# Performance work log

Measured on AMD Instinct MI355X. Metric: run time of the kernel, lower is better.

The kernel has to match this reference:

```python
import jax, jax.numpy as jnp
import numpy as np
import math

HIDDEN = 1024
N_HEADS = 16
HEAD = HIDDEN // N_HEADS

def setup_inputs() -> dict:
    key = jax.random.key(0)
    k1, k2, k3 = jax.random.split(key, 3)
    encodings = jax.random.normal(k1, (2, 2048, HIDDEN), dtype=jnp.float32)
    W_attn = jax.random.normal(k2, (HIDDEN, 3 * HIDDEN), dtype=jnp.float32) * 0.02
    b_attn = jnp.zeros((3 * HIDDEN,), dtype=jnp.float32)
    W_out = jax.random.normal(k3, (HIDDEN, HIDDEN), dtype=jnp.float32) * 0.02
    b_out = jnp.zeros((HIDDEN,), dtype=jnp.float32)
    return {"encodings": encodings, "W_attn": W_attn, "b_attn": b_attn,
            "W_out": W_out, "b_out": b_out}

def reference(encodings, W_attn, b_attn, W_out, b_out):
    b, n, _ = encodings.shape
    qkv = encodings @ W_attn + b_attn              # [b, n, 3*hidden]
    q, k, v = jnp.split(qkv, 3, axis=-1)
    # 'b n (h l) -> b h n l'
    def to_heads(t):
        return t.reshape(b, n, N_HEADS, HEAD).transpose(0, 2, 1, 3)
    q, k, v = to_heads(q), to_heads(k), to_heads(v)
    # scores[b,h,k,q]; causal mask keeps key_pos <= query_pos
    scores = jnp.einsum('bhki,bhqi->bhkq', k, q) / math.sqrt(HEAD)
    mask = jnp.arange(n)[:, None] <= jnp.arange(n)[None, :]   # [k, q]
    scores = jnp.where(mask, scores, jnp.float32(-10000.0))
    attn = jax.nn.softmax(scores, axis=2)          # softmax over key dim
    combined = jnp.einsum('bhkq,bhkl->bhql', attn, v)  # [b, h, n, head]
    out = combined.transpose(0, 2, 1, 3).reshape(b, n, HIDDEN)
    return out @ W_out + b_out
```

## Files before the change

kernel.cpp:

```cpp
#include <hip/hip_runtime.h>
#include <hip/hip_bf16.h>

typedef __attribute__((ext_vector_type(8))) short bf16x8;
typedef __attribute__((ext_vector_type(4))) short bf16x4;
typedef __attribute__((ext_vector_type(4))) float f32x4;

__device__ __forceinline__ short f2bf(float f) {
    unsigned u = __float_as_uint(f);
    u += 0x7fff + ((u >> 16) & 1);
    return (short)(u >> 16);
}
__device__ __forceinline__ float bf2f(short s) {
    return __uint_as_float(((unsigned)(unsigned short)s) << 16);
}
__device__ __forceinline__ unsigned pk_bf16(float lo, float hi) {
    __hip_bfloat162 t = __float22bfloat162_rn(make_float2(lo, hi));
    unsigned u;
    __builtin_memcpy(&u, &t, 4);
    return u;
}

#define GLOAD_LDS16(gp, lp)                                                            \
    __builtin_amdgcn_global_load_lds(                                                  \
        (const __attribute__((address_space(1))) unsigned*)(gp),                       \
        (__attribute__((address_space(3))) unsigned*)(lp), 16, 0, 0)

#define QK_SCALE 0.180336879f
#define MFMA16(a, b, c) __builtin_amdgcn_mfma_f32_16x16x32_bf16((a), (b), (c), 0, 0, 0)

__device__ __forceinline__ void tcvt_tile(const float* __restrict__ W, short* __restrict__ Wt,
                                          int K, int N, int bx, int by, int t,
                                          short (*tile)[72]) {
    const int k0 = by * 64, n0 = bx * 64;
    #pragma unroll
    for (int jj = 0; jj < 4; ++jj) {
        int row = jj * 16 + (t >> 4);
        int col = (t & 15) * 4;
        f32x4 v = *(const f32x4*)&W[(size_t)(k0 + row) * N + n0 + col];
        bf16x4 b = {f2bf(v.x), f2bf(v.y), f2bf(v.z), f2bf(v.w)};
        *(bf16x4*)&tile[row][col] = b;
    }
    __syncthreads();
    const int nr = t >> 2, kc = (t & 3) * 16;
    bf16x8 o0, o1;
    #pragma unroll
    for (int j = 0; j < 8; ++j) { o0[j] = tile[kc + j][nr]; o1[j] = tile[kc + 8 + j][nr]; }
    short* dst = &Wt[(size_t)(n0 + nr) * K + k0 + kc];
    *(bf16x8*)dst = o0;
    *(bf16x8*)(dst + 8) = o1;
}

__global__ __launch_bounds__(256) void prep_kernel(
    const float* __restrict__ enc, const float* __restrict__ Wa,
    const float* __restrict__ ba, const float* __restrict__ Wo,
    const float* __restrict__ bo, short* __restrict__ Abf,
    short* __restrict__ WtA, short* __restrict__ bbA,
    short* __restrict__ WtO, short* __restrict__ bbO)
{
    __shared__ alignas(16) short tile[64][72];
    const int id = blockIdx.x, t = threadIdx.x;
    if (id < 2048) {
        const int i = id * 2048 + t * 8;
        f32x4 a = *(const f32x4*)&enc[i];
        f32x4 b = *(const f32x4*)&enc[i + 4];
        bf16x8 o = {f2bf(a.x), f2bf(a.y), f2bf(a.z), f2bf(a.w),
                    f2bf(b.x), f2bf(b.y), f2bf(b.z), f2bf(b.w)};
        *(bf16x8*)&Abf[i] = o;
    } else if (id == 2048) {
        for (int j = t * 8; j < 3072; j += 2048) {
            f32x4 a = *(const f32x4*)&ba[j];
            f32x4 b = *(const f32x4*)&ba[j + 4];
            bf16x8 o = {f2bf(a.x), f2bf(a.y), f2bf(a.z), f2bf(a.w),
                        f2bf(b.x), f2bf(b.y), f2bf(b.z), f2bf(b.w)};
            *(bf16x8*)&bbA[j] = o;
        }
    } else if (id == 2049) {
        if (t < 128) {
            const int j = t * 8;
            f32x4 a = *(const f32x4*)&bo[j];
            f32x4 b = *(const f32x4*)&bo[j + 4];
            bf16x8 o = {f2bf(a.x), f2bf(a.y), f2bf(a.z), f2bf(a.w),
                        f2bf(b.x), f2bf(b.y), f2bf(b.z), f2bf(b.w)};
            *(bf16x8*)&bbO[j] = o;
        }
        __syncthreads();
    } else if (id < 2818) {
        const int lid = id - 2050;
        tcvt_tile(Wa, WtA, 1024, 3072, lid % 48, lid / 48, t, tile);
    } else {
        const int lid = id - 2818;
        tcvt_tile(Wo, WtO, 1024, 1024, lid % 16, lid / 16, t, tile);
    }
}

template<int BN, bool F32OUT, bool SPLIT3>
__global__ __launch_bounds__(256) void gemm_bt(
    const short* __restrict__ A, const short* __restrict__ Bt,
    const short* __restrict__ bias, void* __restrict__ C,
    short* __restrict__ Kw, short* __restrict__ Vw, int M, int N, int K)
{
    __shared__ alignas(16) short LB[128 * 64 + BN * 64];
    short* As = LB;
    short* Bs = LB + 128 * 64;
    short* Ct = LB;

    const int tid = threadIdx.x, w = tid >> 6, lane = tid & 63;
    const int quad = lane >> 4, l16 = lane & 15;
    constexpr int MT = (BN == 128) ? 4 : 2;
    const int wm = (BN == 128) ? (w >> 1) : w;
    const int wn = (BN == 128) ? (w & 1) : 0;
    const int m0 = blockIdx.y * 128, n0 = blockIdx.x * BN;
    const int srow = lane >> 3;
    const int scol = ((lane & 7) ^ srow) * 8;

    f32x4 acc[MT][4] = {};

    for (int k0 = 0; k0 < K; k0 += 64) {
        __syncthreads();
        #pragma unroll
        for (int jj = 0; jj < 4; ++jj) {
            const int rb = w * 32 + jj * 8;
            GLOAD_LDS16(&A[(size_t)(m0 + rb + srow) * K + k0 + scol], &As[rb * 64]);
        }
        if (BN == 128) {
            #pragma unroll
            for (int jj = 0; jj < 4; ++jj) {
                const int rb = w * 32 + jj * 8;
                GLOAD_LDS16(&Bt[(size_t)(n0 + rb + srow) * K + k0 + scol], &Bs[rb * 64]);
            }
        } else {
            #pragma unroll
            for (int jj = 0; jj < 2; ++jj) {
                const int rb = w * 16 + jj * 8;
                GLOAD_LDS16(&Bt[(size_t)(n0 + rb + srow) * K + k0 + scol], &Bs[rb * 64]);
            }
        }
        __syncthreads();
        #pragma unroll
        for (int half = 0; half < 2; ++half) {
            const int kc2 = half * 4 + quad;
            bf16x8 af[MT], bfr[4];
            #pragma unroll
            for (int i = 0; i < MT; ++i) {
                const int row = wm * (MT * 16) + i * 16 + l16;
                af[i] = *(const bf16x8*)&As[row * 64 + ((kc2 ^ (row & 7)) << 3)];
            }
            #pragma unroll
            for (int i = 0; i < 4; ++i) {
                const int row = wn * 64 + i * 16 + l16;
                bfr[i] = *(const bf16x8*)&Bs[row * 64 + ((kc2 ^ (row & 7)) << 3)];
            }
            #pragma unroll
            for (int mt = 0; mt < MT; ++mt)
                #pragma unroll
                for (int nt = 0; nt < 4; ++nt)
                    acc[mt][nt] = MFMA16(af[mt], bfr[nt], acc[mt][nt]);
        }
    }

    if (SPLIT3) {
        const int g = n0 >> 10;
        const int lc0 = n0 & 1023;
        __syncthreads();
        if (g < 2) {
            #pragma unroll
            for (int nt = 0; nt < 4; ++nt) {
                const int col = wn * 64 + nt * 16 + l16;
                const float bv = bf2f(bias[n0 + col]);
                const int chunk = col >> 3, wi = col & 7;
                #pragma unroll
                for (int mt = 0; mt < 4; ++mt) {
                    const int rbase = wm * 64 + mt * 16 + quad * 4;
                    #pragma unroll
                    for (int r = 0; r < 4; ++r) {
                        const int row = rbase + r;
                        float v = acc[mt][nt][r] + bv;
                        if (g == 0) v *= QK_SCALE;
                        Ct[row * 128 + (((chunk ^ (row & 15)) << 3) | wi)] = f2bf(v);
                    }
                }
            }
        } else {
            #pragma unroll
            for (int nt = 0; nt < 4; ++nt) {
                const int d = wn * 64 + nt * 16 + l16;
                const float bv = bf2f(bias[n0 + d]);
                const int dsw = d & 15;
                #pragma unroll
                for (int mt = 0; mt < 4; ++mt) {
                    const int key0 = wm * 64 + mt * 16 + quad * 4;
                    bf16x4 p = {f2bf(acc[mt][nt][0] + bv), f2bf(acc[mt][nt][1] + bv),
                                f2bf(acc[mt][nt][2] + bv), f2bf(acc[mt][nt][3] + bv)};
                    *(bf16x4*)&Ct[d * 128 + ((((key0 >> 3) ^ dsw) << 3) | (key0 & 7))] = p;
                }
            }
        }
        __syncthreads();
        const int batch = m0 >> 11;
        const int kc0 = (m0 & 2047) >> 6;
        const int head0 = lc0 >> 6;
        if (g == 0) {
            short* dst = (short*)C;
            #pragma unroll
            for (int i = 0; i < 8; ++i) {
                const int idx = i * 256 + tid;
                const int row = idx >> 4, chunk = idx & 15;
                bf16x8 v = *(const bf16x8*)&Ct[row * 128 + ((chunk ^ (row & 15)) << 3)];
                *(bf16x8*)&dst[(size_t)(m0 + row) * 1024 + lc0 + chunk * 8] = v;
            }
        } else if (g == 1) {
            #pragma unroll
            for (int i = 0; i < 8; ++i) {
                const int idx = i * 256 + tid;
                const int qd = idx >> 9, c = idx & 511;
                const int kcL = qd >> 1, headL = qd & 1;
                const int s = c >> 7, h2 = (c >> 6) & 1;
                const int l16c = c & 15, quadc = (c >> 4) & 3;
                const int row = kcL * 64 + s * 16 + l16c;
                const int colc = headL * 8 + h2 * 4 + quadc;
                bf16x8 v = *(const bf16x8*)&Ct[row * 128 + ((colc ^ (row & 15)) << 3)];
                const int bh = batch * 16 + head0 + headL, kc = kc0 + kcL;
                *(bf16x8*)&Kw[((size_t)(bh * 32 + kc) * 512 + c) * 8] = v;
            }
        } else {
            #pragma unroll
            for (int i = 0; i < 8; ++i) {
                const int idx = i * 256 + tid;
                const int qd = idx >> 9, c = idx & 511;
                const int kcL = qd >> 1, headL = qd & 1;
                const int h2 = c >> 8, dt = (c >> 6) & 3;
                const int l16c = c & 15, quadc = (c >> 4) & 3;
                const int d = headL * 64 + dt * 16 + l16c;
                const int keyc = kcL * 8 + h2 * 4 + quadc;
                bf16x8 v = *(const bf16x8*)&Ct[d * 128 + ((keyc ^ (d & 15)) << 3)];
                const int bh = batch * 16 + head0 + headL, kc = kc0 + kcL;
                *(bf16x8*)&Vw[((size_t)(bh * 32 + kc) * 512 + c) * 8] = v;
            }
        }
    } else {
        #pragma unroll
        for (int nt = 0; nt < 4; ++nt) {
            const int col = n0 + wn * 64 + nt * 16 + l16;
            const float bv = bf2f(bias[col]);
            #pragma unroll
            for (int mt = 0; mt < MT; ++mt) {
                const int row = m0 + wm * (MT * 16) + mt * 16 + quad * 4;
                #pragma unroll
                for (int r = 0; r < 4; ++r) {
                    float v = acc[mt][nt][r] + bv;
                    if (F32OUT) ((float*)C)[(size_t)(row + r) * N + col] = v;
                    else        ((short*)C)[(size_t)(row + r) * N + col] = f2bf(v);
                }
            }
        }
    }
}

__global__ __launch_bounds__(256) void attn_kernel(
    const short* __restrict__ Qw, const short* __restrict__ Kx,
    const short* __restrict__ Vx, short* __restrict__ comb)
{
    __shared__ alignas(16) short KV[3][2][4096];
    __shared__ alignas(16) short Ps[4][2][16 * 72];

    const int tid = threadIdx.x, w4 = tid >> 6, lane = tid & 63;
    const int p = w4 >> 1;
    const int w = w4 & 1;
    const int quad = lane >> 4, l16 = lane & 15;
    const int bh = blockIdx.x;
    const int g = blockIdx.y;
    const int tA = 2 * g + p, tB = 63 - tA;
    const int batch = bh >> 4, head = bh & 15;
    const size_t rowbase = (size_t)batch * 2048;
    const int hcol = head * 64;
    const int q0A = tA * 32 + w * 16, q0B = tB * 32 + w * 16;
    const int diagA = g;
    const int maxD = 31 - g;
    const short* Kxbh = Kx + (size_t)bh * 131072;
    const short* Vxbh = Vx + (size_t)bh * 131072;
    const int lofs = lane * 8;
    short* pwA = &Ps[w4][0][0];
    short* pwB = &Ps[w4][1][0];

    bf16x8 qfA[2], qfB[2];
    {
        const short* pa = &Qw[(rowbase + q0A + l16) * 1024 + hcol];
        const short* pb = &Qw[(rowbase + q0B + l16) * 1024 + hcol];
        qfA[0] = *(const bf16x8*)(pa + quad * 8);
        qfA[1] = *(const bf16x8*)(pa + 32 + quad * 8);
        qfB[0] = *(const bf16x8*)(pb + quad * 8);
        qfB[1] = *(const bf16x8*)(pb + 32 + quad * 8);
    }
    asm volatile("s_waitcnt vmcnt(0)" ::: "memory");

    f32x4 otA[4] = {}, otB[4] = {};
    float laccA = 0.f, laccB = 0.f;

    const int sbase = w4 * 64;

    #define STAGE_KV(kcs, buf)                                                              \
        do {                                                                                \
            const size_t nb_ = (size_t)(kcs)*4096;                                          \
            _Pragma("unroll")                                                               \
            for (int j = 0; j < 2; ++j) {                                                   \
                GLOAD_LDS16(&Kxbh[nb_ + (size_t)(j * 256 + sbase + lane) * 8],              \
                            &KV[buf][0][(j * 256 + sbase) * 8]);                            \
                GLOAD_LDS16(&Vxbh[nb_ + (size_t)(j * 256 + sbase + lane) * 8],              \
                            &KV[buf][1][(j * 256 + sbase) * 8]);                            \
            }                                                                               \
        } while (0)

    STAGE_KV(0, 0);
    STAGE_KV(1, 1);
    asm volatile("s_waitcnt vmcnt(4)" ::: "memory");
    __builtin_amdgcn_s_barrier();
    __builtin_amdgcn_sched_barrier(0);

    int cur = 0;
    for (int kc = 0; kc <= maxD; ++kc) {
        const bool actA = (kc <= diagA);
        const int key0 = kc * 64;

        {
            const int ks = (kc + 2 <= maxD) ? kc + 2 : maxD;
            const int wb = (cur + 2 >= 3) ? cur - 1 : cur + 2;
            STAGE_KV(ks, wb);
        }

        bf16x8 kf[4][2];
        #pragma unroll
        for (int s = 0; s < 4; ++s) {
            kf[s][0] = *(const bf16x8*)&KV[cur][0][(s * 2 + 0) * 512 + lofs];
            kf[s][1] = *(const bf16x8*)&KV[cur][0][(s * 2 + 1) * 512 + lofs];
        }

        f32x4 svA[4], svB[4];
        #pragma unroll
        for (int s = 0; s < 4; ++s) {
            f32x4 a = {0.f, 0.f, 0.f, 0.f};
            a = MFMA16(kf[s][0], qfB[0], a);
            a = MFMA16(kf[s][1], qfB[1], a);
            svB[s] = a;
            if (actA) {
                f32x4 b = {0.f, 0.f, 0.f, 0.f};
                b = MFMA16(kf[s][0], qfA[0], b);
                b = MFMA16(kf[s][1], qfA[1], b);
                svA[s] = b;
            }
        }

        bf16x8 vf[2][4];
        #pragma unroll
        for (int hh = 0; hh < 2; ++hh)
            #pragma unroll
            for (int dt = 0; dt < 4; ++dt)
                vf[hh][dt] = *(const bf16x8*)&KV[cur][1][(hh * 4 + dt) * 512 + lofs];

        if (kc == maxD) {
            const int qq = q0B + l16;
            #pragma unroll
            for (int s = 0; s < 4; ++s) {
                const int keyb = key0 + s * 16 + quad * 4;
                #pragma unroll
                for (int r = 0; r < 4; ++r)
                    svB[s][r] = (keyb + r <= qq) ? svB[s][r] : -1e30f;
            }
        }
        #pragma unroll
        for (int s = 0; s < 4; ++s) {
            #pragma unroll
            for (int r = 0; r < 4; ++r) svB[s][r] = exp2f(svB[s][r]);
            laccB += (svB[s][0] + svB[s][1]) + (svB[s][2] + svB[s][3]);
            *(unsigned*)&pwB[l16 * 72 + s * 16 + quad * 4]     = pk_bf16(svB[s][0], svB[s][1]);
            *(unsigned*)&pwB[l16 * 72 + s * 16 + quad * 4 + 2] = pk_bf16(svB[s][2], svB[s][3]);
        }
        if (actA) {
            if (kc == diagA) {
                const int qq = q0A + l16;
                #pragma unroll
                for (int s = 0; s < 4; ++s) {
                    const int keyb = key0 + s * 16 + quad * 4;
                    #pragma unroll
                    for (int r = 0; r < 4; ++r)
                        svA[s][r] = (keyb + r <= qq) ? svA[s][r] : -1e30f;
                }
            }
            #pragma unroll
            for (int s = 0; s < 4; ++s) {
                #pragma unroll
                for (int r = 0; r < 4; ++r) svA[s][r] = exp2f(svA[s][r]);
                laccA += (svA[s][0] + svA[s][1]) + (svA[s][2] + svA[s][3]);
                *(unsigned*)&pwA[l16 * 72 + s * 16 + quad * 4]     = pk_bf16(svA[s][0], svA[s][1]);
                *(unsigned*)&pwA[l16 * 72 + s * 16 + quad * 4 + 2] = pk_bf16(svA[s][2], svA[s][3]);
            }
        }

        {
            bf16x8 pfB0 = *(const bf16x8*)&pwB[l16 * 72 + quad * 8];
            bf16x8 pfB1 = *(const bf16x8*)&pwB[l16 * 72 + 32 + quad * 8];
            #pragma unroll
            for (int dt = 0; dt < 4; ++dt) {
                otB[dt] = MFMA16(vf[0][dt], pfB0, otB[dt]);
                otB[dt] = MFMA16(vf[1][dt], pfB1, otB[dt]);
            }
            if (actA) {
                bf16x8 pfA0 = *(const bf16x8*)&pwA[l16 * 72 + quad * 8];
                bf16x8 pfA1 = *(const bf16x8*)&pwA[l16 * 72 + 32 + quad * 8];
                #pragma unroll
                for (int dt = 0; dt < 4; ++dt) {
                    otA[dt] = MFMA16(vf[0][dt], pfA0, otA[dt]);
                    otA[dt] = MFMA16(vf[1][dt], pfA1, otA[dt]);
                }
            }
        }

        asm volatile("s_waitcnt vmcnt(4)" ::: "memory");
        __builtin_amdgcn_s_barrier();
        __builtin_amdgcn_sched_barrier(0);
        cur = (cur + 1 >= 3) ? 0 : cur + 1;
    }
    #undef STAGE_KV

    laccA += __shfl_xor(laccA, 16);
    laccA += __shfl_xor(laccA, 32);
    laccB += __shfl_xor(laccB, 16);
    laccB += __shfl_xor(laccB, 32);
    const float invA = 1.0f / laccA, invB = 1.0f / laccB;

    #pragma unroll
    for (int dt = 0; dt < 4; ++dt) {
        *(unsigned*)&pwA[l16 * 72 + dt * 16 + quad * 4]     = pk_bf16(otA[dt][0] * invA, otA[dt][1] * invA);
        *(unsigned*)&pwA[l16 * 72 + dt * 16 + quad * 4 + 2] = pk_bf16(otA[dt][2] * invA, otA[dt][3] * invA);
        *(unsigned*)&pwB[l16 * 72 + dt * 16 + quad * 4]     = pk_bf16(otB[dt][0] * invB, otB[dt][1] * invB);
        *(unsigned*)&pwB[l16 * 72 + dt * 16 + quad * 4 + 2] = pk_bf16(otB[dt][2] * invB, otB[dt][3] * invB);
    }
    {
        const int qr = lane >> 2, dc = (lane & 3) * 16;
        bf16x8 a0 = *(const bf16x8*)&pwA[qr * 72 + dc];
        bf16x8 a1 = *(const bf16x8*)&pwA[qr * 72 + dc + 8];
        short* dstA = &comb[(rowbase + q0A + qr) * 1024 + hcol + dc];
        *(bf16x8*)dstA = a0;
        *(bf16x8*)(dstA + 8) = a1;
        bf16x8 b0 = *(const bf16x8*)&pwB[qr * 72 + dc];
        bf16x8 b1 = *(const bf16x8*)&pwB[qr * 72 + dc + 8];
        short* dstB = &comb[(rowbase + q0B + qr) * 1024 + hcol + dc];
        *(bf16x8*)dstB = b0;
        *(bf16x8*)(dstB + 8) = b1;
    }
}

extern "C" void kernel_launch(void* const* d_in, const int* in_sizes, int n_in,
                              void* d_out, int out_size, void* d_ws, size_t ws_size,
                              hipStream_t stream)
{
    const float* enc = (const float*)d_in[0];
    const float* Wa  = (const float*)d_in[1];
    const float* ba  = (const float*)d_in[2];
    const float* Wo  = (const float*)d_in[3];
    const float* bo  = (const float*)d_in[4];
    float* out = (float*)d_out;

    char* ws = (char*)d_ws;
    short* Abf  = (short*)ws;
    short* comb = (short*)ws;
    short* WtO  = (short*)(ws + ((size_t)8 << 20));
    short* bbA  = (short*)(ws + ((size_t)10 << 20));
    short* bbO  = (short*)(ws + ((size_t)10 << 20) + 16384);
    short* WtA  = (short*)(ws + ((size_t)11 << 20));
    short* Kx   = (short*)(ws + ((size_t)17 << 20));
    short* Vx   = (short*)(ws + ((size_t)25 << 20));
    short* Qw   = (short*)(ws + ((size_t)33 << 20));

    prep_kernel<<<3074, 256, 0, stream>>>(enc, Wa, ba, Wo, bo, Abf, WtA, bbA, WtO, bbO);
    gemm_bt<128, false, true><<<dim3(24, 32), 256, 0, stream>>>(
        Abf, WtA, bbA, Qw, Kx, Vx, 4096, 3072, 1024);
    attn_kernel<<<dim3(32, 16), 256, 0, stream>>>(Qw, Kx, Vx, comb);
    gemm_bt<64, true, false><<<dim3(16, 32), 256, 0, stream>>>(
        comb, WtO, bbO, out, nullptr, nullptr, 4096, 1024, 1024);
}
```

Baseline: 189.0 us.

## Keep softmax probabilities in registers instead of an LDS round-trip for PV MFMA

Probabilities are packed to bf16 and fed straight from registers into the PV MFMA, removing the LDS write and read-back through the pw buffers. To make the register layout of P match the MFMA operand, the V staging layout written by the QKV GEMM epilogue is permuted so each 8-element key group gathers two 4-key chunks. This removes LDS traffic and waits in the attention inner loop, at the cost of slightly more scattered LDS reads in the projection epilogue.

Measured after the change: 188.1 us. Within noise of the previous version (-0.5%).

```diff
diff --git a/kernel.cpp b/kernel.cpp
--- a/kernel.cpp
+++ b/kernel.cpp
@@ -231,8 +231,11 @@
                 const int h2 = c >> 8, dt = (c >> 6) & 3;
                 const int l16c = c & 15, quadc = (c >> 4) & 3;
                 const int d = headL * 64 + dt * 16 + l16c;
-                const int keyc = kcL * 8 + h2 * 4 + quadc;
-                bf16x8 v = *(const bf16x8*)&Ct[d * 128 + ((keyc ^ (d & 15)) << 3)];
+                const int Ka = kcL * 64 + h2 * 32 + quadc * 4;
+                const int Kb = Ka + 16;
+                bf16x4 va = *(const bf16x4*)&Ct[d * 128 + (((Ka >> 3) ^ (d & 15)) << 3) + (Ka & 7)];
+                bf16x4 vb = *(const bf16x4*)&Ct[d * 128 + (((Kb >> 3) ^ (d & 15)) << 3) + (Kb & 7)];
+                bf16x8 v = {va[0], va[1], va[2], va[3], vb[0], vb[1], vb[2], vb[3]};
                 const int bh = batch * 16 + head0 + headL, kc = kc0 + kcL;
                 *(bf16x8*)&Vw[((size_t)(bh * 32 + kc) * 512 + c) * 8] = v;
             }
@@ -366,14 +369,30 @@
                     svB[s][r] = (keyb + r <= qq) ? svB[s][r] : -1e30f;
             }
         }
-        #pragma unroll
-        for (int s = 0; s < 4; ++s) {
-            #pragma unroll
-            for (int r = 0; r < 4; ++r) svB[s][r] = exp2f(svB[s][r]);
-            laccB += (svB[s][0] + svB[s][1]) + (svB[s][2] + svB[s][3]);
-            *(unsigned*)&pwB[l16 * 72 + s * 16 + quad * 4]     = pk_bf16(svB[s][0], svB[s][1]);
-            *(unsigned*)&pwB[l16 * 72 + s * 16 + quad * 4 + 2] = pk_bf16(svB[s][2], svB[s][3]);
-        }
+        {
+            unsigned uB[4][2];
+            #pragma unroll
+            for (int s = 0; s < 4; ++s) {
+                #pragma unroll
+                for (int r = 0; r < 4; ++r) svB[s][r] = exp2f(svB[s][r]);
+                laccB += (svB[s][0] + svB[s][1]) + (svB[s][2] + svB[s][3]);
+                uB[s][0] = pk_bf16(svB[s][0], svB[s][1]);
+                uB[s][1] = pk_bf16(svB[s][2], svB[s][3]);
+            }
+            bf16x8 pfB0, pfB1;
+            {
+                unsigned t0[4] = {uB[0][0], uB[0][1], uB[1][0], uB[1][1]};
+                unsigned t1[4] = {uB[2][0], uB[2][1], uB[3][0], uB[3][1]};
+                __builtin_memcpy(&pfB0, t0, 16);
+                __builtin_memcpy(&pfB1, t1, 16);
+            }
+            #pragma unroll
+            for (int dt = 0; dt < 4; ++dt) {
+                otB[dt] = MFMA16(vf[0][dt], pfB0, otB[dt]);
+                otB[dt] = MFMA16(vf[1][dt], pfB1, otB[dt]);
+            }
+        }
+
         if (actA) {
             if (kc == diagA) {
                 const int qq = q0A + l16;
@@ -385,32 +404,26 @@
                         svA[s][r] = (keyb + r <= qq) ? svA[s][r] : -1e30f;
                 }
             }
+            unsigned uA[4][2];
             #pragma unroll
             for (int s = 0; s < 4; ++s) {
                 #pragma unroll
                 for (int r = 0; r < 4; ++r) svA[s][r] = exp2f(svA[s][r]);
                 laccA += (svA[s][0] + svA[s][1]) + (svA[s][2] + svA[s][3]);
-                *(unsigned*)&pwA[l16 * 72 + s * 16 + quad * 4]     = pk_bf16(svA[s][0], svA[s][1]);
-                *(unsigned*)&pwA[l16 * 72 + s * 16 + quad * 4 + 2] = pk_bf16(svA[s][2], svA[s][3]);
-            }
-        }
-
-        {
-            bf16x8 pfB0 = *(const bf16x8*)&pwB[l16 * 72 + quad * 8];
-            bf16x8 pfB1 = *(const bf16x8*)&pwB[l16 * 72 + 32 + quad * 8];
+                uA[s][0] = pk_bf16(svA[s][0], svA[s][1]);
+                uA[s][1] = pk_bf16(svA[s][2], svA[s][3]);
+            }
+            bf16x8 pfA0, pfA1;
+            {
+                unsigned t0[4] = {uA[0][0], uA[0][1], uA[1][0], uA[1][1]};
+                unsigned t1[4] = {uA[2][0], uA[2][1], uA[3][0], uA[3][1]};
+                __builtin_memcpy(&pfA0, t0, 16);
+                __builtin_memcpy(&pfA1, t1, 16);
+            }
             #pragma unroll
             for (int dt = 0; dt < 4; ++dt) {
-                otB[dt] = MFMA16(vf[0][dt], pfB0, otB[dt]);
-                otB[dt] = MFMA16(vf[1][dt], pfB1, otB[dt]);
-            }
-            if (actA) {
-                bf16x8 pfA0 = *(const bf16x8*)&pwA[l16 * 72 + quad * 8];
-                bf16x8 pfA1 = *(const bf16x8*)&pwA[l16 * 72 + 32 + quad * 8];
-                #pragma unroll
-                for (int dt = 0; dt < 4; ++dt) {
-                    otA[dt] = MFMA16(vf[0][dt], pfA0, otA[dt]);
-                    otA[dt] = MFMA16(vf[1][dt], pfA1, otA[dt]);
-                }
+                otA[dt] = MFMA16(vf[0][dt], pfA0, otA[dt]);
+                otA[dt] = MFMA16(vf[1][dt], pfA1, otA[dt]);
             }
         }
 
```

## Repack V layout so P stays in registers; one 64-row query tile per block

Applied to the files above, without the earlier changes.

The V workspace layout written by the QKV GEMM epilogue is permuted so the exp'd score fragments can serve directly as the B operand of the PV MFMA. This removes the per-iteration LDS round-trip for P. The attention kernel also drops the paired-tile (A/B) causal load balancing in favor of 1024 blocks, each handling one 64-query tile, scheduled longest-first. The final output staging reuses the KV shared buffer, cutting LDS footprint to help occupancy, at the cost of more blocks and less K/V reuse per staged chunk.

New measurement: 178.4 us. -5.6%, faster.

```diff
diff --git a/kernel.cpp b/kernel.cpp
--- a/kernel.cpp
+++ b/kernel.cpp
@@ -231,8 +231,11 @@
                 const int h2 = c >> 8, dt = (c >> 6) & 3;
                 const int l16c = c & 15, quadc = (c >> 4) & 3;
                 const int d = headL * 64 + dt * 16 + l16c;
-                const int keyc = kcL * 8 + h2 * 4 + quadc;
-                bf16x8 v = *(const bf16x8*)&Ct[d * 128 + ((keyc ^ (d & 15)) << 3)];
+                const int Ka = kcL * 64 + h2 * 32 + quadc * 4;
+                const int Kb = Ka + 16;
+                bf16x4 va = *(const bf16x4*)&Ct[d * 128 + (((Ka >> 3) ^ (d & 15)) << 3) + (Ka & 7)];
+                bf16x4 vb = *(const bf16x4*)&Ct[d * 128 + (((Kb >> 3) ^ (d & 15)) << 3) + (Kb & 7)];
+                bf16x8 v = {va[0], va[1], va[2], va[3], vb[0], vb[1], vb[2], vb[3]};
                 const int bh = batch * 16 + head0 + headL, kc = kc0 + kcL;
                 *(bf16x8*)&Vw[((size_t)(bh * 32 + kc) * 512 + c) * 8] = v;
             }
@@ -261,40 +264,30 @@
     const short* __restrict__ Vx, short* __restrict__ comb)
 {
     __shared__ alignas(16) short KV[3][2][4096];
-    __shared__ alignas(16) short Ps[4][2][16 * 72];
 
     const int tid = threadIdx.x, w4 = tid >> 6, lane = tid & 63;
-    const int p = w4 >> 1;
-    const int w = w4 & 1;
     const int quad = lane >> 4, l16 = lane & 15;
-    const int bh = blockIdx.x;
-    const int g = blockIdx.y;
-    const int tA = 2 * g + p, tB = 63 - tA;
+    const int blk = blockIdx.x;
+    const int n = 31 - (blk >> 5);
+    const int bh = blk & 31;
     const int batch = bh >> 4, head = bh & 15;
     const size_t rowbase = (size_t)batch * 2048;
     const int hcol = head * 64;
-    const int q0A = tA * 32 + w * 16, q0B = tB * 32 + w * 16;
-    const int diagA = g;
-    const int maxD = 31 - g;
+    const int q0 = n * 64 + w4 * 16;
     const short* Kxbh = Kx + (size_t)bh * 131072;
     const short* Vxbh = Vx + (size_t)bh * 131072;
     const int lofs = lane * 8;
-    short* pwA = &Ps[w4][0][0];
-    short* pwB = &Ps[w4][1][0];
-
-    bf16x8 qfA[2], qfB[2];
+
+    bf16x8 qf[2];
     {
-        const short* pa = &Qw[(rowbase + q0A + l16) * 1024 + hcol];
-        const short* pb = &Qw[(rowbase + q0B + l16) * 1024 + hcol];
-        qfA[0] = *(const bf16x8*)(pa + quad * 8);
-        qfA[1] = *(const bf16x8*)(pa + 32 + quad * 8);
-        qfB[0] = *(const bf16x8*)(pb + quad * 8);
-        qfB[1] = *(const bf16x8*)(pb + 32 + quad * 8);
+        const short* pq = &Qw[(rowbase + q0 + l16) * 1024 + hcol];
+        qf[0] = *(const bf16x8*)(pq + quad * 8);
+        qf[1] = *(const bf16x8*)(pq + 32 + quad * 8);
     }
     asm volatile("s_waitcnt vmcnt(0)" ::: "memory");
 
-    f32x4 otA[4] = {}, otB[4] = {};
-    float laccA = 0.f, laccB = 0.f;
+    f32x4 ot[4] = {};
+    float lacc = 0.f;
 
     const int sbase = w4 * 64;
 
@@ -311,18 +304,15 @@
         } while (0)
 
     STAGE_KV(0, 0);
-    STAGE_KV(1, 1);
+    STAGE_KV((n >= 1) ? 1 : 0, 1);
     asm volatile("s_waitcnt vmcnt(4)" ::: "memory");
     __builtin_amdgcn_s_barrier();
     __builtin_amdgcn_sched_barrier(0);
 
     int cur = 0;
-    for (int kc = 0; kc <= maxD; ++kc) {
-        const bool actA = (kc <= diagA);
-        const int key0 = kc * 64;
-
+    for (int kc = 0; kc <= n; ++kc) {
         {
-            const int ks = (kc + 2 <= maxD) ? kc + 2 : maxD;
+            const int ks = (kc + 2 <= n) ? kc + 2 : n;
             const int wb = (cur + 2 >= 3) ? cur - 1 : cur + 2;
             STAGE_KV(ks, wb);
         }
@@ -334,19 +324,13 @@
             kf[s][1] = *(const bf16x8*)&KV[cur][0][(s * 2 + 1) * 512 + lofs];
         }
 
-        f32x4 svA[4], svB[4];
+        f32x4 sv[4];
         #pragma unroll
         for (int s = 0; s < 4; ++s) {
             f32x4 a = {0.f, 0.f, 0.f, 0.f};
-            a = MFMA16(kf[s][0], qfB[0], a);
-            a = MFMA16(kf[s][1], qfB[1], a);
-            svB[s] = a;
-            if (actA) {
-                f32x4 b = {0.f, 0.f, 0.f, 0.f};
-                b = MFMA16(kf[s][0], qfA[0], b);
-                b = MFMA16(kf[s][1], qfA[1], b);
-                svA[s] = b;
-            }
+            a = MFMA16(kf[s][0], qf[0], a);
+            a = MFMA16(kf[s][1], qf[1], a);
+            sv[s] = a;
         }
 
         bf16x8 vf[2][4];
@@ -356,61 +340,37 @@
             for (int dt = 0; dt < 4; ++dt)
                 vf[hh][dt] = *(const bf16x8*)&KV[cur][1][(hh * 4 + dt) * 512 + lofs];
 
-        if (kc == maxD) {
-            const int qq = q0B + l16;
+        if (kc == n) {
+            const int qq = q0 + l16;
             #pragma unroll
             for (int s = 0; s < 4; ++s) {
-                const int keyb = key0 + s * 16 + quad * 4;
+                const int keyb = kc * 64 + s * 16 + quad * 4;
                 #pragma unroll
                 for (int r = 0; r < 4; ++r)
-                    svB[s][r] = (keyb + r <= qq) ? svB[s][r] : -1e30f;
-            }
-        }
-        #pragma unroll
-        for (int s = 0; s < 4; ++s) {
-            #pragma unroll
-            for (int r = 0; r < 4; ++r) svB[s][r] = exp2f(svB[s][r]);
-            laccB += (svB[s][0] + svB[s][1]) + (svB[s][2] + svB[s][3]);
-            *(unsigned*)&pwB[l16 * 72 + s * 16 + quad * 4]     = pk_bf16(svB[s][0], svB[s][1]);
-            *(unsigned*)&pwB[l16 * 72 + s * 16 + quad * 4 + 2] = pk_bf16(svB[s][2], svB[s][3]);
-        }
-        if (actA) {
-            if (kc == diagA) {
-                const int qq = q0A + l16;
-                #pragma unroll
-                for (int s = 0; s < 4; ++s) {
-                    const int keyb = key0 + s * 16 + quad * 4;
-                    #pragma unroll
-                    for (int r = 0; r < 4; ++r)
-                        svA[s][r] = (keyb + r <= qq) ? svA[s][r] : -1e30f;
-                }
-            }
+                    sv[s][r] = (keyb + r <= qq) ? sv[s][r] : -1e30f;
+            }
+        }
+        {
+            unsigned u[4][2];
             #pragma unroll
             for (int s = 0; s < 4; ++s) {
                 #pragma unroll
-                for (int r = 0; r < 4; ++r) svA[s][r] = exp2f(svA[s][r]);
-                laccA += (svA[s][0] + svA[s][1]) + (svA[s][2] + svA[s][3]);
-                *(unsigned*)&pwA[l16 * 72 + s * 16 + quad * 4]     = pk_bf16(svA[s][0], svA[s][1]);
-                *(unsigned*)&pwA[l16 * 72 + s * 16 + quad * 4 + 2] = pk_bf16(svA[s][2], svA[s][3]);
-            }
-        }
-
-        {
-            bf16x8 pfB0 = *(const bf16x8*)&pwB[l16 * 72 + quad * 8];
-            bf16x8 pfB1 = *(const bf16x8*)&pwB[l16 * 72 + 32 + quad * 8];
+                for (int r = 0; r < 4; ++r) sv[s][r] = exp2f(sv[s][r]);
+                lacc += (sv[s][0] + sv[s][1]) + (sv[s][2] + sv[s][3]);
+                u[s][0] = pk_bf16(sv[s][0], sv[s][1]);
+                u[s][1] = pk_bf16(sv[s][2], sv[s][3]);
+            }
+            bf16x8 pf0, pf1;
+            {
+                unsigned t0[4] = {u[0][0], u[0][1], u[1][0], u[1][1]};
+                unsigned t1[4] = {u[2][0], u[2][1], u[3][0], u[3][1]};
+                __builtin_memcpy(&pf0, t0, 16);
+                __builtin_memcpy(&pf1, t1, 16);
+            }
             #pragma unroll
             for (int dt = 0; dt < 4; ++dt) {
-                otB[dt] = MFMA16(vf[0][dt], pfB0, otB[dt]);
-                otB[dt] = MFMA16(vf[1][dt], pfB1, otB[dt]);
-            }
-            if (actA) {
-                bf16x8 pfA0 = *(const bf16x8*)&pwA[l16 * 72 + quad * 8];
-                bf16x8 pfA1 = *(const bf16x8*)&pwA[l16 * 72 + 32 + quad * 8];
-                #pragma unroll
-                for (int dt = 0; dt < 4; ++dt) {
-                    otA[dt] = MFMA16(vf[0][dt], pfA0, otA[dt]);
-                    otA[dt] = MFMA16(vf[1][dt], pfA1, otA[dt]);
-                }
+                ot[dt] = MFMA16(vf[0][dt], pf0, ot[dt]);
+                ot[dt] = MFMA16(vf[1][dt], pf1, ot[dt]);
             }
         }
 
@@ -421,31 +381,26 @@
     }
     #undef STAGE_KV
 
-    laccA += __shfl_xor(laccA, 16);
-    laccA += __shfl_xor(laccA, 32);
-    laccB += __shfl_xor(laccB, 16);
-    laccB += __shfl_xor(laccB, 32);
-    const float invA = 1.0f / laccA, invB = 1.0f / laccB;
-
+    asm volatile("s_waitcnt vmcnt(0)" ::: "memory");
+    __builtin_amdgcn_s_barrier();
+
+    lacc += __shfl_xor(lacc, 16);
+    lacc += __shfl_xor(lacc, 32);
+    const float inv = 1.0f / lacc;
+
+    short* pw = &KV[0][0][0] + w4 * 1152;
     #pragma unroll
     for (int dt = 0; dt < 4; ++dt) {
-        *(unsigned*)&pwA[l16 * 72 + dt * 16 + quad * 4]     = pk_bf16(otA[dt][0] * invA, otA[dt][1] * invA);
-        *(unsigned*)&pwA[l16 * 72 + dt * 16 + quad * 4 + 2] = pk_bf16(otA[dt][2] * invA, otA[dt][3] * invA);
-        *(unsigned*)&pwB[l16 * 72 + dt * 16 + quad * 4]     = pk_bf16(otB[dt][0] * invB, otB[dt][1] * invB);
-        *(unsigned*)&pwB[l16 * 72 + dt * 16 + quad * 4 + 2] = pk_bf16(otB[dt][2] * invB, otB[dt][3] * invB);
+        *(unsigned*)&pw[l16 * 72 + dt * 16 + quad * 4]     = pk_bf16(ot[dt][0] * inv, ot[dt][1] * inv);
+        *(unsigned*)&pw[l16 * 72 + dt * 16 + quad * 4 + 2] = pk_bf16(ot[dt][2] * inv, ot[dt][3] * inv);
     }
     {
         const int qr = lane >> 2, dc = (lane & 3) * 16;
-        bf16x8 a0 = *(const bf16x8*)&pwA[qr * 72 + dc];
-        bf16x8 a1 = *(const bf16x8*)&pwA[qr * 72 + dc + 8];
-        short* dstA = &comb[(rowbase + q0A + qr) * 1024 + hcol + dc];
-        *(bf16x8*)dstA = a0;
-        *(bf16x8*)(dstA + 8) = a1;
-        bf16x8 b0 = *(const bf16x8*)&pwB[qr * 72 + dc];
-        bf16x8 b1 = *(const bf16x8*)&pwB[qr * 72 + dc + 8];
-        short* dstB = &comb[(rowbase + q0B + qr) * 1024 + hcol + dc];
-        *(bf16x8*)dstB = b0;
-        *(bf16x8*)(dstB + 8) = b1;
+        bf16x8 a0 = *(const bf16x8*)&pw[qr * 72 + dc];
+        bf16x8 a1 = *(const bf16x8*)&pw[qr * 72 + dc + 8];
+        short* dst = &comb[(rowbase + q0 + qr) * 1024 + hcol + dc];
+        *(bf16x8*)dst = a0;
+        *(bf16x8*)(dst + 8) = a1;
     }
 }
 
@@ -474,7 +429,7 @@
     prep_kernel<<<3074, 256, 0, stream>>>(enc, Wa, ba, Wo, bo, Abf, WtA, bbA, WtO, bbO);
     gemm_bt<128, false, true><<<dim3(24, 32), 256, 0, stream>>>(
         Abf, WtA, bbA, Qw, Kx, Vx, 4096, 3072, 1024);
-    attn_kernel<<<dim3(32, 16), 256, 0, stream>>>(Qw, Kx, Vx, comb);
+    attn_kernel<<<1024, 256, 0, stream>>>(Qw, Kx, Vx, comb);
     gemm_bt<64, true, false><<<dim3(16, 32), 256, 0, stream>>>(
         comb, WtO, bbO, out, nullptr, nullptr, 4096, 1024, 1024);
 }
```
